# Kernel optimization log

Measured on AMD Instinct MI355X. Metric: run time of the kernel, lower is better.

The kernel has to match this reference:

```python
import jax, jax.numpy as jnp
import numpy as np

N_MICRO = 500_000
MICRO_DIM = 512
MACRO_DIM = 512
N_NODES = 20_000
N_EDGES = 40_000
EPS_SOFTMAX = 1e-8
EPS_LN = 1e-5


def setup_inputs() -> dict:
    key = jax.random.key(0)
    k = jax.random.split(key, 8)
    micro_features = jax.random.normal(k[0], (N_MICRO, MICRO_DIM), dtype=jnp.float32)
    # raw in [0, N_NODES+N_EDGES+2000): first N_NODES -> node ids, next N_EDGES -> edges
    # (encoded as -id-1), rest -> -100 (ignored)
    raw = jax.random.randint(k[1], (N_MICRO,), 0, N_NODES + N_EDGES + 2000)
    micro_to_macro = jnp.where(
        raw < N_NODES, raw,
        jnp.where(raw < N_NODES + N_EDGES, -(raw - N_NODES) - 1, -100)
    ).astype(jnp.int32)
    attn_w = jax.random.normal(k[2], (MICRO_DIM,), dtype=jnp.float32) / np.sqrt(MICRO_DIM)
    attn_b = jnp.zeros((), dtype=jnp.float32)
    proj_w = jax.random.normal(k[3], (MICRO_DIM, MACRO_DIM), dtype=jnp.float32) / np.sqrt(MICRO_DIM)
    proj_b = jnp.zeros((MACRO_DIM,), dtype=jnp.float32)
    ln_g = jnp.ones((MACRO_DIM,), dtype=jnp.float32)
    ln_b = jnp.zeros((MACRO_DIM,), dtype=jnp.float32)
    return {
        "micro_features": micro_features,
        "attn_w": attn_w, "attn_b": attn_b,
        "proj_w": proj_w, "proj_b": proj_b,
        "ln_g": ln_g, "ln_b": ln_b,
        "micro_to_macro": micro_to_macro,
        "num_macro_nodes": N_NODES,
        "num_macro_edges": N_EDGES,
    }


def _segment_softmax(logits, idx, num_segments):
    m = jax.ops.segment_max(logits, idx, num_segments=num_segments)
    e = jnp.exp(logits - m[idx])
    s = jax.ops.segment_sum(e, idx, num_segments=num_segments) + EPS_SOFTMAX
    return e / s[idx]


def reference(micro_features, attn_w, attn_b, proj_w, proj_b, ln_g, ln_b,
              micro_to_macro, num_macro_nodes, num_macro_edges):
    # per-element attention logit (Linear(micro_dim, 1))
    logits = micro_features @ attn_w + attn_b  # [N]

    node_mask = micro_to_macro >= 0
    edge_mask = (micro_to_macro < 0) & (micro_to_macro != -100)

    def aggregate(mapped_idx, mask, nseg):
        # route masked-out elements to a dummy trailing segment, dropped at the end
        idx = jnp.where(mask, mapped_idx, nseg)
        w = _segment_softmax(logits, idx, nseg + 1)  # [N]
        agg = jax.ops.segment_sum(micro_features * w[:, None], idx, num_segments=nseg + 1)
        return agg[:nseg]  # [nseg, micro_dim]

    node_agg = aggregate(micro_to_macro, node_mask, num_macro_nodes)
    edge_agg = aggregate(-micro_to_macro - 1, edge_mask, num_macro_edges)

    def out_proj(x):
        h = x @ proj_w + proj_b
        mu = jnp.mean(h, axis=-1, keepdims=True)
        var = jnp.mean(jnp.square(h - mu), axis=-1, keepdims=True)
        ln = (h - mu) / jnp.sqrt(var + EPS_LN) * ln_g + ln_b
        return jax.nn.gelu(ln, approximate=False)  # torch GELU default = exact erf

    return out_proj(node_agg), out_proj(edge_agg)
```

## Files before the change

kernel.cpp:

```cpp
#include <hip/hip_runtime.h>
#include <hip/hip_bf16.h>
#include <math.h>

#define N_NODES 20000
#define N_EDGES 40000
#define N_SEG   (N_NODES + N_EDGES)
#define CAP     64
#define DIM     512

typedef __attribute__((ext_vector_type(8))) short short8;
typedef __attribute__((ext_vector_type(4))) float floatx4;

__device__ __forceinline__ unsigned short f2b(float f) {
    union { float f; unsigned int i; } v; v.f = f;
    unsigned int i = v.i;
    unsigned int r = (i + 0x7fffu + ((i >> 16) & 1u)) >> 16;
    return (unsigned short)r;
}

__global__ __launch_bounds__(256) void k_front(
    const float* __restrict__ feat,
    const float* __restrict__ attn_w,
    const float* __restrict__ attn_b,
    const int* __restrict__ m2m,
    const float* __restrict__ W,
    float* __restrict__ seg_sum,
    int* __restrict__ seg_cnt,
    int* __restrict__ perm,
    float* __restrict__ eperm,
    unsigned short* __restrict__ Wt,
    int n_micro, int nbl)
{
    __shared__ float tile[64][68];
    int t = threadIdx.x;

    if (blockIdx.x >= (unsigned)nbl) {
        int b = blockIdx.x - nbl;
        int bx = b & 7, by = b >> 3;
        int r0 = by * 64, c0 = bx * 64;
#pragma unroll
        for (int i = 0; i < 4; ++i) {
            int idx = i * 256 + t;
            int r = idx >> 4, ch = (idx & 15) * 4;
            *(float4*)&tile[r][ch] = *(const float4*)&W[(size_t)(r0 + r) * 512 + c0 + ch];
        }
        __syncthreads();
#pragma unroll
        for (int i = 0; i < 2; ++i) {
            int idx = i * 256 + t;
            int n = idx >> 3, kc = (idx & 7) * 8;
            union { unsigned short us[8]; uint4 v; } o;
#pragma unroll
            for (int j = 0; j < 8; ++j) o.us[j] = f2b(tile[kc + j][n]);
            *(uint4*)&Wt[(size_t)(c0 + n) * 512 + r0 + kc] = o.v;
        }
        return;
    }

    int lane = t & 63;
    int row0 = (blockIdx.x * 4 + (t >> 6)) * 2;
    if (row0 >= n_micro) return;
    bool has1 = (row0 + 1) < n_micro;

    float4 w0 = *(const float4*)&attn_w[lane * 8];
    float4 w1 = *(const float4*)&attn_w[lane * 8 + 4];

    const float* fr0 = &feat[(size_t)row0 * DIM + lane * 8];
    float4 a0 = *(const float4*)fr0;
    float4 a1 = *(const float4*)(fr0 + 4);
    float4 b0 = make_float4(0, 0, 0, 0), b1 = make_float4(0, 0, 0, 0);
    if (has1) {
        b0 = *(const float4*)(fr0 + DIM);
        b1 = *(const float4*)(fr0 + DIM + 4);
    }

    float p0 = 0.f, p1 = 0.f;
    p0 = fmaf(a0.x, w0.x, p0); p0 = fmaf(a0.y, w0.y, p0);
    p0 = fmaf(a0.z, w0.z, p0); p0 = fmaf(a0.w, w0.w, p0);
    p0 = fmaf(a1.x, w1.x, p0); p0 = fmaf(a1.y, w1.y, p0);
    p0 = fmaf(a1.z, w1.z, p0); p0 = fmaf(a1.w, w1.w, p0);
    p1 = fmaf(b0.x, w0.x, p1); p1 = fmaf(b0.y, w0.y, p1);
    p1 = fmaf(b0.z, w0.z, p1); p1 = fmaf(b0.w, w0.w, p1);
    p1 = fmaf(b1.x, w1.x, p1); p1 = fmaf(b1.y, w1.y, p1);
    p1 = fmaf(b1.z, w1.z, p1); p1 = fmaf(b1.w, w1.w, p1);
#pragma unroll
    for (int d = 32; d > 0; d >>= 1) {
        p0 += __shfl_xor(p0, d);
        p1 += __shfl_xor(p1, d);
    }

    if ((lane & 31) == 0) {
        int row = row0 + (lane >> 5);
        if (row < n_micro) {
            float pv = (lane == 0) ? p0 : p1;
            float e = expf(pv + attn_b[0]);
            int m = m2m[row];
            int seg = -1;
            if (m >= 0) seg = m;
            else if (m != -100) seg = N_NODES + (-m - 1);
            if (seg >= 0) {
                atomicAdd(&seg_sum[seg], e);
                int pos = atomicAdd(&seg_cnt[seg], 1);
                if (pos < CAP) {
                    perm[seg * CAP + pos]  = row;
                    eperm[seg * CAP + pos] = e;
                }
            }
        }
    }
}

__global__ __launch_bounds__(256) void k_agg(
    const float* __restrict__ feat,
    const float* __restrict__ seg_sum,
    const int* __restrict__ seg_cnt,
    const int* __restrict__ perm,
    const float* __restrict__ eperm,
    unsigned short* __restrict__ agg)
{
    int lane = threadIdx.x & 63;
    int seg  = blockIdx.x * 4 + (threadIdx.x >> 6);
    if (seg >= N_SEG) return;

    int cnt = seg_cnt[seg];
    if (cnt > CAP) cnt = CAP;
    float sinv = 1.0f / (seg_sum[seg] + 1e-8f);

    int   myidx = (lane < cnt) ? perm[seg * CAP + lane]  : 0;
    float mye   = (lane < cnt) ? eperm[seg * CAP + lane] : 0.f;

    float acc[8] = {0.f, 0.f, 0.f, 0.f, 0.f, 0.f, 0.f, 0.f};
    float4 c0 = make_float4(0, 0, 0, 0), c1 = make_float4(0, 0, 0, 0);
    if (cnt > 0) {
        int i0 = __shfl(myidx, 0);
        const float* fr = &feat[(size_t)i0 * DIM + lane * 8];
        c0 = *(const float4*)fr; c1 = *(const float4*)(fr + 4);
    }
    for (int j = 0; j < cnt; ++j) {
        float4 n0 = c0, n1 = c1;
        if (j + 1 < cnt) {
            int i1 = __shfl(myidx, j + 1);
            const float* fr = &feat[(size_t)i1 * DIM + lane * 8];
            n0 = *(const float4*)fr; n1 = *(const float4*)(fr + 4);
        }
        float w = __shfl(mye, j) * sinv;
        acc[0] = fmaf(w, c0.x, acc[0]); acc[1] = fmaf(w, c0.y, acc[1]);
        acc[2] = fmaf(w, c0.z, acc[2]); acc[3] = fmaf(w, c0.w, acc[3]);
        acc[4] = fmaf(w, c1.x, acc[4]); acc[5] = fmaf(w, c1.y, acc[5]);
        acc[6] = fmaf(w, c1.z, acc[6]); acc[7] = fmaf(w, c1.w, acc[7]);
        c0 = n0; c1 = n1;
    }
    union { unsigned short us[8]; uint4 v; } o;
#pragma unroll
    for (int k = 0; k < 8; ++k) o.us[k] = f2b(acc[k]);
    *(uint4*)&agg[(size_t)seg * DIM + lane * 8] = o.v;
}

__global__ __launch_bounds__(256, 2) void k_proj(
    const unsigned short* __restrict__ A,
    const unsigned short* __restrict__ Wt,
    const float* __restrict__ pb,
    const float* __restrict__ lg,
    const float* __restrict__ lb,
    float* __restrict__ out)
{
    __shared__ union {
        struct { unsigned short a[64 * 40]; unsigned short b[512 * 40]; } st;
        struct { float h[16 * 516]; float ps[16][17]; float ps2[16][17];
                 float mu[16]; float rs[16]; } ep;
    } u;

    int t = threadIdx.x;
    int w = t >> 6, lane = t & 63;
    int quad = lane >> 4, l15 = lane & 15;
    int bm0 = blockIdx.x * 64;

    floatx4 acc[4][8];
#pragma unroll
    for (int mt = 0; mt < 4; ++mt)
#pragma unroll
        for (int nt = 0; nt < 8; ++nt)
            acc[mt][nt] = (floatx4){0.f, 0.f, 0.f, 0.f};

    for (int kk = 0; kk < 512; kk += 32) {
        {
            int r = t >> 2, k8 = (t & 3) * 8;
            *(uint4*)&u.st.a[r * 40 + k8] = *(const uint4*)&A[(size_t)(bm0 + r) * 512 + kk + k8];
        }
#pragma unroll
        for (int i = 0; i < 8; ++i) {
            int c = i * 256 + t;
            int n = c >> 2, k8 = (c & 3) * 8;
            *(uint4*)&u.st.b[n * 40 + k8] = *(const uint4*)&Wt[(size_t)n * 512 + kk + k8];
        }
        __syncthreads();

        int kb = quad * 8;
        short8 af[4], bf[8];
#pragma unroll
        for (int mt = 0; mt < 4; ++mt)
            af[mt] = *(const short8*)&u.st.a[(mt * 16 + l15) * 40 + kb];
#pragma unroll
        for (int nt = 0; nt < 8; ++nt)
            bf[nt] = *(const short8*)&u.st.b[(w * 128 + nt * 16 + l15) * 40 + kb];
#pragma unroll
        for (int mt = 0; mt < 4; ++mt)
#pragma unroll
            for (int nt = 0; nt < 8; ++nt)
                acc[mt][nt] = __builtin_amdgcn_mfma_f32_16x16x32_bf16(af[mt], bf[nt], acc[mt][nt], 0, 0, 0);
        __syncthreads();
    }

#pragma unroll 1
    for (int mt = 0; mt < 4; ++mt) {
        if (bm0 + mt * 16 >= N_SEG) break;
        __syncthreads();
#pragma unroll
        for (int nt = 0; nt < 8; ++nt) {
            int col = w * 128 + nt * 16 + l15;
            float pbv = pb[col];
#pragma unroll
            for (int r = 0; r < 4; ++r) {
                int row = quad * 4 + r;
                u.ep.h[row * 516 + col] = acc[mt][nt][r] + pbv;
            }
        }
        __syncthreads();

        {
            int row = t & 15, part = t >> 4;
            float s = 0.f, s2 = 0.f;
#pragma unroll
            for (int c4 = 0; c4 < 8; ++c4) {
                float4 v = *(const float4*)&u.ep.h[row * 516 + part * 32 + c4 * 4];
                s  += v.x + v.y + v.z + v.w;
                s2 += v.x * v.x + v.y * v.y + v.z * v.z + v.w * v.w;
            }
            u.ep.ps[part][row]  = s;
            u.ep.ps2[part][row] = s2;
        }
        __syncthreads();
        if (t < 16) {
            float S = 0.f, S2 = 0.f;
#pragma unroll
            for (int p = 0; p < 16; ++p) { S += u.ep.ps[p][t]; S2 += u.ep.ps2[p][t]; }
            float mu  = S * (1.0f / 512.0f);
            float var = S2 * (1.0f / 512.0f) - mu * mu;
            u.ep.mu[t] = mu;
            u.ep.rs[t] = rsqrtf(fmaxf(var, 0.f) + 1e-5f);
        }
        __syncthreads();

#pragma unroll
        for (int i = 0; i < 8; ++i) {
            int c = i * 256 + t;
            int r = c >> 7, c4 = (c & 127) * 4;
            float4 v = *(const float4*)&u.ep.h[r * 516 + c4];
            float mu = u.ep.mu[r], rs = u.ep.rs[r];
            float vv[4] = {v.x, v.y, v.z, v.w};
            float4 o;
            float* op = &o.x;
#pragma unroll
            for (int j = 0; j < 4; ++j) {
                float x = (vv[j] - mu) * rs * lg[c4 + j] + lb[c4 + j];
                op[j] = 0.5f * x * (1.0f + erff(x * 0.70710678118f));
            }
            *(float4*)&out[(size_t)(bm0 + mt * 16 + r) * 512 + c4] = o;
        }
    }
}

extern "C" void kernel_launch(void* const* d_in, const int* in_sizes, int n_in,
                              void* d_out, int out_size, void* d_ws, size_t ws_size,
                              hipStream_t stream)
{
    const float* feat   = (const float*)d_in[0];
    const float* attn_w = (const float*)d_in[1];
    const float* attn_b = (const float*)d_in[2];
    const float* proj_w = (const float*)d_in[3];
    const float* proj_b = (const float*)d_in[4];
    const float* ln_g   = (const float*)d_in[5];
    const float* ln_b   = (const float*)d_in[6];
    const int*   m2m    = (const int*)d_in[7];
    float* out          = (float*)d_out;

    int n_micro = in_sizes[0] / DIM;

    char* ws = (char*)d_ws;
    float* seg_sum = (float*)ws;
    int*   seg_cnt = (int*)(seg_sum + N_SEG);
    int*   perm    = seg_cnt + N_SEG;
    float* eperm   = (float*)(perm + (size_t)N_SEG * CAP);
    unsigned short* Wt  = (unsigned short*)(eperm + (size_t)N_SEG * CAP);
    unsigned short* agg = Wt + 512 * 512;

    int nbl = (n_micro + 7) / 8;

    hipMemsetAsync(seg_sum, 0, (size_t)N_SEG * 2 * sizeof(float), stream);
    k_front<<<nbl + 64, 256, 0, stream>>>(feat, attn_w, attn_b, m2m, proj_w,
                                          seg_sum, seg_cnt, perm, eperm, Wt,
                                          n_micro, nbl);
    k_agg<<<(N_SEG + 3) / 4, 256, 0, stream>>>(feat, seg_sum, seg_cnt, perm, eperm, agg);
    k_proj<<<(N_SEG + 63) / 64, 256, 0, stream>>>(agg, Wt, proj_b, ln_g, ln_b, out);
    (void)n_in; (void)out_size; (void)ws_size;
}
```

Measured before the change: 1.950 ms.

## Fuse attention logit computation into the segment aggregation pass

The front kernel no longer reads every feature row to compute logits and accumulate per-segment exp sums with atomics. It now only buckets row indices per segment. The aggregation kernel computes each row's logit with a wave-wide dot product and shuffle reduction as it loads the row, accumulating exp-weighted features and the exp sum locally, then normalizes at the end. This removes a full pass over the feature matrix, the float atomics and the eperm storage. In exchange, each step of the serial per-segment loop now carries a dependent shuffle reduction and an exp, which lengthens the chain inside the loop.

Measured after the change: 1.781 ms. -8.7%, faster.

```diff
diff --git a/kernel.cpp b/kernel.cpp
--- a/kernel.cpp
+++ b/kernel.cpp
@@ -19,15 +19,10 @@
 }
 
 __global__ __launch_bounds__(256) void k_front(
-    const float* __restrict__ feat,
-    const float* __restrict__ attn_w,
-    const float* __restrict__ attn_b,
     const int* __restrict__ m2m,
     const float* __restrict__ W,
-    float* __restrict__ seg_sum,
     int* __restrict__ seg_cnt,
     int* __restrict__ perm,
-    float* __restrict__ eperm,
     unsigned short* __restrict__ Wt,
     int n_micro, int nbl)
 {
@@ -57,65 +52,24 @@
         return;
     }
 
-    int lane = t & 63;
-    int row0 = (blockIdx.x * 4 + (t >> 6)) * 2;
-    if (row0 >= n_micro) return;
-    bool has1 = (row0 + 1) < n_micro;
-
-    float4 w0 = *(const float4*)&attn_w[lane * 8];
-    float4 w1 = *(const float4*)&attn_w[lane * 8 + 4];
-
-    const float* fr0 = &feat[(size_t)row0 * DIM + lane * 8];
-    float4 a0 = *(const float4*)fr0;
-    float4 a1 = *(const float4*)(fr0 + 4);
-    float4 b0 = make_float4(0, 0, 0, 0), b1 = make_float4(0, 0, 0, 0);
-    if (has1) {
-        b0 = *(const float4*)(fr0 + DIM);
-        b1 = *(const float4*)(fr0 + DIM + 4);
-    }
-
-    float p0 = 0.f, p1 = 0.f;
-    p0 = fmaf(a0.x, w0.x, p0); p0 = fmaf(a0.y, w0.y, p0);
-    p0 = fmaf(a0.z, w0.z, p0); p0 = fmaf(a0.w, w0.w, p0);
-    p0 = fmaf(a1.x, w1.x, p0); p0 = fmaf(a1.y, w1.y, p0);
-    p0 = fmaf(a1.z, w1.z, p0); p0 = fmaf(a1.w, w1.w, p0);
-    p1 = fmaf(b0.x, w0.x, p1); p1 = fmaf(b0.y, w0.y, p1);
-    p1 = fmaf(b0.z, w0.z, p1); p1 = fmaf(b0.w, w0.w, p1);
-    p1 = fmaf(b1.x, w1.x, p1); p1 = fmaf(b1.y, w1.y, p1);
-    p1 = fmaf(b1.z, w1.z, p1); p1 = fmaf(b1.w, w1.w, p1);
-#pragma unroll
-    for (int d = 32; d > 0; d >>= 1) {
-        p0 += __shfl_xor(p0, d);
-        p1 += __shfl_xor(p1, d);
-    }
-
-    if ((lane & 31) == 0) {
-        int row = row0 + (lane >> 5);
-        if (row < n_micro) {
-            float pv = (lane == 0) ? p0 : p1;
-            float e = expf(pv + attn_b[0]);
-            int m = m2m[row];
-            int seg = -1;
-            if (m >= 0) seg = m;
-            else if (m != -100) seg = N_NODES + (-m - 1);
-            if (seg >= 0) {
-                atomicAdd(&seg_sum[seg], e);
-                int pos = atomicAdd(&seg_cnt[seg], 1);
-                if (pos < CAP) {
-                    perm[seg * CAP + pos]  = row;
-                    eperm[seg * CAP + pos] = e;
-                }
-            }
-        }
+    int row = blockIdx.x * 256 + t;
+    if (row >= n_micro) return;
+    int m = m2m[row];
+    int seg = -1;
+    if (m >= 0) seg = m;
+    else if (m != -100) seg = N_NODES + (-m - 1);
+    if (seg >= 0) {
+        int pos = atomicAdd(&seg_cnt[seg], 1);
+        if (pos < CAP) perm[seg * CAP + pos] = row;
     }
 }
 
 __global__ __launch_bounds__(256) void k_agg(
     const float* __restrict__ feat,
-    const float* __restrict__ seg_sum,
+    const float* __restrict__ attn_w,
+    const float* __restrict__ attn_b,
     const int* __restrict__ seg_cnt,
     const int* __restrict__ perm,
-    const float* __restrict__ eperm,
     unsigned short* __restrict__ agg)
 {
     int lane = threadIdx.x & 63;
@@ -124,12 +78,15 @@
 
     int cnt = seg_cnt[seg];
     if (cnt > CAP) cnt = CAP;
-    float sinv = 1.0f / (seg_sum[seg] + 1e-8f);
-
-    int   myidx = (lane < cnt) ? perm[seg * CAP + lane]  : 0;
-    float mye   = (lane < cnt) ? eperm[seg * CAP + lane] : 0.f;
+
+    float4 w0 = *(const float4*)&attn_w[lane * 8];
+    float4 w1 = *(const float4*)&attn_w[lane * 8 + 4];
+    float ab = attn_b[0];
+
+    int myidx = (lane < cnt) ? perm[seg * CAP + lane] : 0;
 
     float acc[8] = {0.f, 0.f, 0.f, 0.f, 0.f, 0.f, 0.f, 0.f};
+    float ssum = 0.f;
     float4 c0 = make_float4(0, 0, 0, 0), c1 = make_float4(0, 0, 0, 0);
     if (cnt > 0) {
         int i0 = __shfl(myidx, 0);
@@ -143,16 +100,25 @@
             const float* fr = &feat[(size_t)i1 * DIM + lane * 8];
             n0 = *(const float4*)fr; n1 = *(const float4*)(fr + 4);
         }
-        float w = __shfl(mye, j) * sinv;
-        acc[0] = fmaf(w, c0.x, acc[0]); acc[1] = fmaf(w, c0.y, acc[1]);
-        acc[2] = fmaf(w, c0.z, acc[2]); acc[3] = fmaf(w, c0.w, acc[3]);
-        acc[4] = fmaf(w, c1.x, acc[4]); acc[5] = fmaf(w, c1.y, acc[5]);
-        acc[6] = fmaf(w, c1.z, acc[6]); acc[7] = fmaf(w, c1.w, acc[7]);
+        float p = 0.f;
+        p = fmaf(c0.x, w0.x, p); p = fmaf(c0.y, w0.y, p);
+        p = fmaf(c0.z, w0.z, p); p = fmaf(c0.w, w0.w, p);
+        p = fmaf(c1.x, w1.x, p); p = fmaf(c1.y, w1.y, p);
+        p = fmaf(c1.z, w1.z, p); p = fmaf(c1.w, w1.w, p);
+#pragma unroll
+        for (int d = 32; d > 0; d >>= 1) p += __shfl_xor(p, d);
+        float e = expf(p + ab);
+        ssum += e;
+        acc[0] = fmaf(e, c0.x, acc[0]); acc[1] = fmaf(e, c0.y, acc[1]);
+        acc[2] = fmaf(e, c0.z, acc[2]); acc[3] = fmaf(e, c0.w, acc[3]);
+        acc[4] = fmaf(e, c1.x, acc[4]); acc[5] = fmaf(e, c1.y, acc[5]);
+        acc[6] = fmaf(e, c1.z, acc[6]); acc[7] = fmaf(e, c1.w, acc[7]);
         c0 = n0; c1 = n1;
     }
+    float sinv = 1.0f / (ssum + 1e-8f);
     union { unsigned short us[8]; uint4 v; } o;
 #pragma unroll
-    for (int k = 0; k < 8; ++k) o.us[k] = f2b(acc[k]);
+    for (int k = 0; k < 8; ++k) o.us[k] = f2b(acc[k] * sinv);
     *(uint4*)&agg[(size_t)seg * DIM + lane * 8] = o.v;
 }
 
@@ -287,20 +253,16 @@
     int n_micro = in_sizes[0] / DIM;
 
     char* ws = (char*)d_ws;
-    float* seg_sum = (float*)ws;
-    int*   seg_cnt = (int*)(seg_sum + N_SEG);
+    int*   seg_cnt = (int*)ws;
     int*   perm    = seg_cnt + N_SEG;
-    float* eperm   = (float*)(perm + (size_t)N_SEG * CAP);
-    unsigned short* Wt  = (unsigned short*)(eperm + (size_t)N_SEG * CAP);
+    unsigned short* Wt  = (unsigned short*)(perm + (size_t)N_SEG * CAP);
     unsigned short* agg = Wt + 512 * 512;
 
-    int nbl = (n_micro + 7) / 8;
-
-    hipMemsetAsync(seg_sum, 0, (size_t)N_SEG * 2 * sizeof(float), stream);
-    k_front<<<nbl + 64, 256, 0, stream>>>(feat, attn_w, attn_b, m2m, proj_w,
-                                          seg_sum, seg_cnt, perm, eperm, Wt,
-                                          n_micro, nbl);
-    k_agg<<<(N_SEG + 3) / 4, 256, 0, stream>>>(feat, seg_sum, seg_cnt, perm, eperm, agg);
+    int nbl = (n_micro + 255) / 256;
+
+    hipMemsetAsync(seg_cnt, 0, (size_t)N_SEG * sizeof(int), stream);
+    k_front<<<nbl + 64, 256, 0, stream>>>(m2m, proj_w, seg_cnt, perm, Wt, n_micro, nbl);
+    k_agg<<<(N_SEG + 3) / 4, 256, 0, stream>>>(feat, attn_w, attn_b, seg_cnt, perm, agg);
     k_proj<<<(N_SEG + 63) / 64, 256, 0, stream>>>(agg, Wt, proj_b, ln_g, ln_b, out);
     (void)n_in; (void)out_size; (void)ws_size;
 }
```
